# Optimization experiments

Measured on AMD Instinct MI355X. Metric: run time of the kernel, lower is better.

Reference implementation:

```python
import jax, jax.numpy as jnp
import numpy as np

HID = 64
NUM_LAYER = 3
N_OBJ = 100000
N_P1, N_P2, N_P3 = 200000, 400000, 200000
NUM_GRAPHS = 256


def _mlp(x, w1, b1, w2, b2):
    # pyg.nn.MLP([in, hid, out], norm=None): Linear -> ReLU -> Linear
    return jnp.dot(jax.nn.relu(jnp.dot(x, w1) + b1), w2) + b2


def _gather(obj, ei):
    # ei: [arity, n_atoms] object index per argument slot
    r, n = ei.shape
    g = jnp.take(obj, ei, axis=0)  # [r, n, HID]
    return jnp.moveaxis(g, 0, 1).reshape(n, r * HID)  # concat per-position embeddings


def _scatter(atom, ei, n_obj):
    # split atom embedding [n, r*HID] into r chunks and scatter-add to objects
    r, n = ei.shape
    chunks = jnp.moveaxis(atom.reshape(n, r, HID), 1, 0).reshape(r * n, HID)
    return jax.ops.segment_sum(chunks, ei.reshape(-1), num_segments=n_obj)


def _lin_init(key, fan_in, fan_out):
    kw, kb = jax.random.split(key)
    w = jax.random.normal(kw, (fan_in, fan_out), jnp.float32) / np.float32(np.sqrt(fan_in))
    b = jax.random.normal(kb, (fan_out,), jnp.float32) * 0.01
    return w, b


def setup_inputs() -> dict:
    key = jax.random.key(0)
    ks = jax.random.split(key, 16)
    inp = {}
    inp["x_obj"] = jnp.zeros((N_OBJ, 1), jnp.float32)
    inp["x_p1"] = jnp.zeros((N_P1, 1), jnp.float32)
    inp["x_p2"] = jnp.zeros((N_P2, 2), jnp.float32)
    inp["x_p3"] = jnp.zeros((N_P3, 3), jnp.float32)
    for i, (name, r) in enumerate([("p1", 1), ("p2", 2), ("p3", 3)]):
        d = HID * r
        w1, b1 = _lin_init(ks[2 * i], d, d)
        w2, b2 = _lin_init(ks[2 * i + 1], d, d)
        inp[f"w_{name}_1"], inp[f"b_{name}_1"] = w1, b1
        inp[f"w_{name}_2"], inp[f"b_{name}_2"] = w2, b2
    inp["w_u1"], inp["b_u1"] = _lin_init(ks[6], 2 * HID, 2 * HID)
    inp["w_u2"], inp["b_u2"] = _lin_init(ks[7], 2 * HID, HID)
    inp["w_r1"], inp["b_r1"] = _lin_init(ks[8], HID, 2 * HID)
    inp["w_r2"], inp["b_r2"] = _lin_init(ks[9], 2 * HID, 1)
    inp["ei_p1"] = jax.random.randint(ks[10], (1, N_P1), 0, N_OBJ, jnp.int32)
    inp["ei_p2"] = jax.random.randint(ks[11], (2, N_P2), 0, N_OBJ, jnp.int32)
    inp["ei_p3"] = jax.random.randint(ks[12], (3, N_P3), 0, N_OBJ, jnp.int32)
    inp["batch_obj"] = jnp.sort(jax.random.randint(ks[13], (N_OBJ,), 0, NUM_GRAPHS, jnp.int32))
    inp["num_graphs"] = NUM_GRAPHS
    return inp


def reference(x_obj, x_p1, x_p2, x_p3,
              w_p1_1, b_p1_1, w_p1_2, b_p1_2,
              w_p2_1, b_p2_1, w_p2_2, b_p2_2,
              w_p3_1, b_p3_1, w_p3_2, b_p3_2,
              w_u1, b_u1, w_u2, b_u2,
              w_r1, b_r1, w_r2, b_r2,
              ei_p1, ei_p2, ei_p3, batch_obj, num_graphs):
    n_obj = x_obj.shape[0]
    # encoding_layer: everything starts at zeros of size [N, F*hidden]
    obj = jnp.zeros((n_obj, x_obj.shape[1] * HID), jnp.float32)
    for _ in range(NUM_LAYER):
        # FanOutMP: gather arg-object embeddings, per-predicate MLP -> atom embeddings
        a1 = _mlp(_gather(obj, ei_p1), w_p1_1, b_p1_1, w_p1_2, b_p1_2)
        a2 = _mlp(_gather(obj, ei_p2), w_p2_1, b_p2_1, w_p2_2, b_p2_2)
        a3 = _mlp(_gather(obj, ei_p3), w_p3_1, b_p3_1, w_p3_2, b_p3_2)
        # FanInMP: split atom emb into arity chunks, scatter-add back to objects
        agg = (_scatter(a1, ei_p1, n_obj) + _scatter(a2, ei_p2, n_obj)
               + _scatter(a3, ei_p3, n_obj))
        # obj_update on cat([old_obj, aggregated])
        obj = _mlp(jnp.concatenate([obj, agg], axis=1), w_u1, b_u1, w_u2, b_u2)
    # global_add_pool + readout
    pooled = jax.ops.segment_sum(obj, batch_obj, num_segments=num_graphs)
    return _mlp(pooled, w_r1, b_r1, w_r2, b_r2).reshape(-1)
```

## Files before the change

kernel.cpp:

```cpp
#include <hip/hip_runtime.h>
#include <hip/hip_fp16.h>

typedef _Float16 h8 __attribute__((ext_vector_type(8)));
typedef float f32x4 __attribute__((ext_vector_type(4)));

__device__ __forceinline__ f32x4 mfma2(h8 ah, h8 bh, h8 bl, f32x4 c) {
    c = __builtin_amdgcn_mfma_f32_16x16x32_f16(ah, bh, c, 0, 0, 0);
    c = __builtin_amdgcn_mfma_f32_16x16x32_f16(ah, bl, c, 0, 0, 0);
    return c;
}

__launch_bounds__(256)
__global__ void wprep(const float* __restrict__ w_p1_1, const float* __restrict__ w_p1_2,
                      const float* __restrict__ w_p2_1, const float* __restrict__ w_p2_2,
                      const float* __restrict__ w_p3_1, const float* __restrict__ w_p3_2,
                      const float* __restrict__ w_u1, const float* __restrict__ w_u2,
                      _Float16* __restrict__ hb)
{
    int b = blockIdx.x;
    const float* src; int K, N, base; size_t off;
    if      (b < 16)  { src = w_p1_1; K = 64;  N = 64;  base = 0;   off = 0;      }
    else if (b < 32)  { src = w_p1_2; K = 64;  N = 64;  base = 16;  off = 8192;   }
    else if (b < 96)  { src = w_p2_1; K = 128; N = 128; base = 32;  off = 16384;  }
    else if (b < 160) { src = w_p2_2; K = 128; N = 128; base = 96;  off = 49152;  }
    else if (b < 304) { src = w_p3_1; K = 192; N = 192; base = 160; off = 81920;  }
    else if (b < 448) { src = w_p3_2; K = 192; N = 192; base = 304; off = 155648; }
    else if (b < 512) { src = w_u1;   K = 128; N = 128; base = 448; off = 229376; }
    else              { src = w_u2;   K = 128; N = 64;  base = 512; off = 262144; }
    int e = (b - base) * 256 + threadIdx.x;
    if (e < K * N) {
        int n = e / K, k = e - n * K;
        float x = src[k * N + n];
        _Float16 h = (_Float16)x;
        hb[off + e] = h;
        hb[off + (size_t)K * N + e] = (_Float16)(x - (float)h);
    }
}

__launch_bounds__(256)
__global__ void aconst_k(const float* __restrict__ b_p1_1, const float* __restrict__ w_p1_2,
                         const float* __restrict__ b_p1_2,
                         const float* __restrict__ b_p2_1, const float* __restrict__ w_p2_2,
                         const float* __restrict__ b_p2_2,
                         const float* __restrict__ b_p3_1, const float* __restrict__ w_p3_2,
                         const float* __restrict__ b_p3_2,
                         float* __restrict__ ac)
{
    int p = blockIdx.x;
    const float *b1, *w2, *b2; int D, off;
    if      (p == 0) { b1 = b_p1_1; w2 = w_p1_2; b2 = b_p1_2; D = 64;  off = 0;   }
    else if (p == 1) { b1 = b_p2_1; w2 = w_p2_2; b2 = b_p2_2; D = 128; off = 64;  }
    else             { b1 = b_p3_1; w2 = w_p3_2; b2 = b_p3_2; D = 192; off = 192; }
    int n = threadIdx.x;
    if (n < D) {
        float s = b2[n];
        for (int k = 0; k < D; ++k) {
            float h = b1[k];
            h = h > 0.f ? h : 0.f;
            s = fmaf(h, w2[k * D + n], s);
        }
        ac[off + n] = s;
    }
}

__launch_bounds__(256)
__global__ void hist_k(const int* __restrict__ ei1, const int* __restrict__ ei2,
                       const int* __restrict__ ei3, int* __restrict__ counts,
                       int n_obj, int n1, int n2, int n3)
{
    int e = blockIdx.x * 256 + threadIdx.x;
    int t1 = n1, t2 = n1 + 2 * n2, t3 = t2 + 3 * n3;
    int o, j;
    if (e < t1) { o = ei1[e]; j = 0; }
    else if (e < t2) { int x = e - t1; o = ei2[x]; j = 1 + (x >= n2 ? 1 : 0); }
    else if (e < t3) { int y = e - t2; o = ei3[y]; j = 3 + (y >= n3 ? 1 : 0) + (y >= 2 * n3 ? 1 : 0); }
    else return;
    atomicAdd(&counts[(size_t)j * n_obj + o], 1);
    atomicAdd(&counts[(size_t)6 * n_obj + o], 1);
}

__launch_bounds__(1024)
__global__ void scan_k(const int* __restrict__ deg, int* __restrict__ rowptr,
                       int* __restrict__ cursor, int n)
{
    __shared__ int buf[1024];
    __shared__ int carry_s;
    int tid = threadIdx.x;
    if (tid == 0) carry_s = 0;
    __syncthreads();
    for (int base = 0; base < n; base += 4096) {
        int idx = base + tid * 4;
        int v[4];
#pragma unroll
        for (int k = 0; k < 4; ++k) { int i = idx + k; v[k] = (i < n) ? deg[i] : 0; }
        int tsum = v[0] + v[1] + v[2] + v[3];
        buf[tid] = tsum;
        __syncthreads();
        for (int off = 1; off < 1024; off <<= 1) {
            int t = (tid >= off) ? buf[tid - off] : 0;
            __syncthreads();
            buf[tid] += t;
            __syncthreads();
        }
        int run = buf[tid] - tsum + carry_s;
#pragma unroll
        for (int k = 0; k < 4; ++k) {
            int i = idx + k;
            if (i < n) { rowptr[i] = run; cursor[i] = run; }
            run += v[k];
        }
        __syncthreads();
        if (tid == 1023) carry_s += buf[1023];
        __syncthreads();
    }
    if (tid == 0) rowptr[n] = carry_s;
}

__launch_bounds__(256)
__global__ void fill_k(const int* __restrict__ ei1, const int* __restrict__ ei2,
                       const int* __restrict__ ei3, int* __restrict__ cursor,
                       int* __restrict__ epos, int n1, int n2, int n3)
{
    int e = blockIdx.x * 256 + threadIdx.x;
    int t1 = n1, t2 = n1 + 2 * n2, t3 = t2 + 3 * n3;
    int o;
    if (e < t1) o = ei1[e];
    else if (e < t2) o = ei2[e - t1];
    else if (e < t3) o = ei3[e - t2];
    else return;
    epos[e] = atomicAdd(&cursor[o], 1);
}

__launch_bounds__(256)
__global__ void bcast_k(const int* __restrict__ counts, const float* __restrict__ ac,
                        _Float16* __restrict__ aggh, int n_obj)
{
    __shared__ float ch[384];
    int tid = threadIdx.x;
    for (int i = tid; i < 384; i += 256) ch[i] = ac[i];
    __syncthreads();
    int i = blockIdx.x * 256 + tid;
    int o = i >> 3, q = i & 7;
    if (o < n_obj) {
        float c[6];
#pragma unroll
        for (int j = 0; j < 6; ++j) c[j] = (float)counts[(size_t)j * n_obj + o];
        h8 v;
#pragma unroll
        for (int comp = 0; comp < 8; ++comp) {
            int col = 8 * q + comp;
            float s = 0.f;
#pragma unroll
            for (int j = 0; j < 6; ++j) s = fmaf(c[j], ch[j * 64 + col], s);
            v[comp] = (_Float16)s;
        }
        *(h8*)(aggh + (size_t)o * 64 + 8 * q) = v;
    }
}

template<int R, int STORE>
__device__ __forceinline__ void pred_body(
    char* smem,
    const _Float16* __restrict__ objh, const int* __restrict__ ei,
    const int* __restrict__ epos, int cbase,
    const _Float16* __restrict__ W1h, const _Float16* __restrict__ W1l,
    const float* __restrict__ B1,
    const _Float16* __restrict__ W2h, const _Float16* __restrict__ W2l,
    const float* __restrict__ B2,
    _Float16* __restrict__ aggh, _Float16* __restrict__ chunks,
    int n_atoms, int blk)
{
    constexpr int D = 64 * R;
    constexpr int KC = D / 32;
    constexpr int LDA = D + 8;
    _Float16* Ah = (_Float16*)smem;
    int* eis = (int*)(Ah + 64 * LDA);

    const int tid = threadIdx.x;
    const int wave = tid >> 6, lane = tid & 63;
    const int r = lane & 15, g = lane >> 4;
    const int a_base = blk * 64;
    const int tb = wave * R;

    for (int i = tid; i < R * 64; i += 256) {
        int s = i >> 6, a = i & 63;
        int ag = a_base + a; if (ag >= n_atoms) ag = n_atoms - 1;
        eis[i] = ei[s * n_atoms + ag];
    }
    __syncthreads();
    {
        h8 vv[2 * R];
#pragma unroll
        for (int i = 0; i < 2 * R; ++i) {
            int f = tid + 256 * i;
            int rowslot = f >> 3, c = f & 7;
            int s = rowslot >> 6, a = rowslot & 63;
            vv[i] = *(const h8*)(objh + (size_t)eis[s * 64 + a] * 64 + c * 8);
        }
#pragma unroll
        for (int i = 0; i < 2 * R; ++i) {
            int f = tid + 256 * i;
            int rowslot = f >> 3, c = f & 7;
            int s = rowslot >> 6, a = rowslot & 63;
            *(h8*)(Ah + a * LDA + s * 64 + c * 8) = vv[i];
        }
    }
    __syncthreads();

    f32x4 z = {0.f, 0.f, 0.f, 0.f};
    f32x4 acc[4][R];
#pragma unroll
    for (int rt = 0; rt < 4; ++rt)
#pragma unroll
        for (int t = 0; t < R; ++t) acc[rt][t] = z;

    {
        h8 bh[2][R], bl[2][R];
#pragma unroll
        for (int t = 0; t < R; ++t) {
            size_t wo = (size_t)((tb + t) * 16 + r) * D + g * 8;
            bh[0][t] = *(const h8*)(W1h + wo);
            bl[0][t] = *(const h8*)(W1l + wo);
        }
#pragma unroll
        for (int kc = 0; kc < KC; ++kc) {
            const int cur = kc & 1, nxt = cur ^ 1;
            if (kc + 1 < KC) {
#pragma unroll
                for (int t = 0; t < R; ++t) {
                    size_t wo = (size_t)((tb + t) * 16 + r) * D + (kc + 1) * 32 + g * 8;
                    bh[nxt][t] = *(const h8*)(W1h + wo);
                    bl[nxt][t] = *(const h8*)(W1l + wo);
                }
            }
            const int ko = kc * 32 + g * 8;
            h8 ah[4];
#pragma unroll
            for (int rt = 0; rt < 4; ++rt)
                ah[rt] = *(const h8*)(Ah + (rt * 16 + r) * LDA + ko);
// ... 71 lines not shown
                    int row = rt * 16 + g * 4 + q;
                    Ah[row * LDA + s * 64 + cc] = (_Float16)(acc[rt][t][q] + b2);
                }
        }
        __syncthreads();
#pragma unroll
        for (int p = 0; p < 2 * R; ++p) {
            int i = p * 32 + (tid >> 3);
            int s = i >> 6, a = i & 63;
            int c8 = tid & 7;
            int atom = a_base + a;
            if (atom < n_atoms) {
                int pos = epos[cbase + s * n_atoms + atom];
                *(h8*)(chunks + (size_t)pos * 64 + c8 * 8) =
                    *(const h8*)(Ah + a * LDA + s * 64 + c8 * 8);
            }
        }
    } else {
#pragma unroll
        for (int t = 0; t < R; ++t) {
            int col = (tb + t) * 16 + r;
            float b2 = B2[col];
            int s = col >> 6, cc = col & 63;
#pragma unroll
            for (int rt = 0; rt < 4; ++rt)
#pragma unroll
                for (int q = 0; q < 4; ++q) {
                    int row = rt * 16 + g * 4 + q;
                    int atom = a_base + row;
                    float v = acc[rt][t][q] + b2;
                    float v2 = __shfl_xor(v, 1);
                    if (atom < n_atoms && (r & 1) == 0) {
                        __half2 hv = __floats2half2_rn(v, v2);
                        unsafeAtomicAdd((__half2*)(aggh + (size_t)eis[s * 64 + row] * 64 + cc), hv);
                    }
                }
        }
    }
}

template<int STORE>
__launch_bounds__(256, 6)
__global__ void pred_all(const _Float16* __restrict__ objh, _Float16* __restrict__ aggh,
                         _Float16* __restrict__ chunks, const int* __restrict__ epos,
                         const int* __restrict__ ei1, const int* __restrict__ ei2,
                         const int* __restrict__ ei3,
                         const _Float16* __restrict__ hb,
                         const float* __restrict__ b_p1_1, const float* __restrict__ b_p1_2,
                         const float* __restrict__ b_p2_1, const float* __restrict__ b_p2_2,
                         const float* __restrict__ b_p3_1, const float* __restrict__ b_p3_2,
                         int n1, int n2, int n3, int nb3, int nb2)
{
    extern __shared__ char smem[];
    int b = blockIdx.x;
    if (b < nb3) {
        pred_body<3, STORE>(smem, objh, ei3, epos, n1 + 2 * n2,
                            hb + 81920, hb + 118784, b_p3_1,
                            hb + 155648, hb + 192512, b_p3_2, aggh, chunks, n3, b);
    } else if (b < nb3 + nb2) {
        pred_body<2, STORE>(smem, objh, ei2, epos, n1,
                            hb + 16384, hb + 32768, b_p2_1,
                            hb + 49152, hb + 65536, b_p2_2, aggh, chunks, n2, b - nb3);
    } else {
        pred_body<1, STORE>(smem, objh, ei1, epos, 0,
                            hb + 0, hb + 4096, b_p1_1,
                            hb + 8192, hb + 12288, b_p1_2, aggh, chunks, n1, b - nb3 - nb2);
    }
}

__launch_bounds__(256, 4)
__global__ void fanin_update(_Float16* __restrict__ objh,
                             const _Float16* __restrict__ chunks,
                             const int* __restrict__ rowptr,
                             const _Float16* __restrict__ W1h, const _Float16* __restrict__ W1l,
                             const float* __restrict__ B1,
                             const _Float16* __restrict__ W2h, const _Float16* __restrict__ W2l,
                             const float* __restrict__ B2,
                             int n_obj, int last, float* __restrict__ aggf)
{
    constexpr int LDA = 136;
    __shared__ _Float16 Ah[64 * LDA];

    const int tid = threadIdx.x;
    const int wave = tid >> 6, lane = tid & 63;
    const int r = lane & 15, g = lane >> 4;
    const int a_base = blockIdx.x * 64;

    const int o_local = tid >> 2, part = tid & 3;
    const int o = a_base + o_local;
    const bool valid = o < n_obj;
    const int b = valid ? rowptr[o] : 0;
    const int e2 = valid ? rowptr[o + 1] : 0;
    float s[16];
#pragma unroll
    for (int j = 0; j < 16; ++j) s[j] = 0.f;
    for (int i = b; i < e2; ++i) {
        const h8* cp = (const h8*)(chunks + (size_t)i * 64 + part * 16);
        h8 v0 = cp[0], v1 = cp[1];
#pragma unroll
        for (int j = 0; j < 8; ++j) { s[j] += (float)v0[j]; s[8 + j] += (float)v1[j]; }
    }
    {
        int oc = valid ? o : n_obj - 1;
        h8 u0 = *(const h8*)(objh + (size_t)oc * 64 + part * 16);
        h8 u1 = *(const h8*)(objh + (size_t)oc * 64 + part * 16 + 8);
        *(h8*)(Ah + o_local * LDA + part * 16) = u0;
        *(h8*)(Ah + o_local * LDA + part * 16 + 8) = u1;
        h8 a0, a1;
#pragma unroll
        for (int j = 0; j < 8; ++j) { a0[j] = (_Float16)s[j]; a1[j] = (_Float16)s[8 + j]; }
        *(h8*)(Ah + o_local * LDA + 64 + part * 16) = a0;
        *(h8*)(Ah + o_local * LDA + 64 + part * 16 + 8) = a1;
    }
    __syncthreads();

    f32x4 z = {0.f, 0.f, 0.f, 0.f};
    f32x4 acc[4][2];
#pragma unroll
    for (int rt = 0; rt < 4; ++rt) { acc[rt][0] = z; acc[rt][1] = z; }
    {
        h8 bh[2][2], bl[2][2];
#pragma unroll
        for (int t = 0; t < 2; ++t) {
            size_t wo = (size_t)((wave * 2 + t) * 16 + r) * 128 + g * 8;
            bh[0][t] = *(const h8*)(W1h + wo);
            bl[0][t] = *(const h8*)(W1l + wo);
        }
#pragma unroll
        for (int kc = 0; kc < 4; ++kc) {
            const int cur = kc & 1, nxt = cur ^ 1;
            if (kc + 1 < 4) {
#pragma unroll
                for (int t = 0; t < 2; ++t) {
                    size_t wo = (size_t)((wave * 2 + t) * 16 + r) * 128 + (kc + 1) * 32 + g * 8;
                    bh[nxt][t] = *(const h8*)(W1h + wo);
                    bl[nxt][t] = *(const h8*)(W1l + wo);
                }
            }
            const int ko = kc * 32 + g * 8;
            h8 ah[4];
#pragma unroll
            for (int rt = 0; rt < 4; ++rt)
                ah[rt] = *(const h8*)(Ah + (rt * 16 + r) * LDA + ko);
#pragma unroll
            for (int t = 0; t < 2; ++t)
#pragma unroll
                for (int rt = 0; rt < 4; ++rt)
                    acc[rt][t] = mfma2(ah[rt], bh[cur][t], bl[cur][t], acc[rt][t]);
        }
    }
    __syncthreads();
#pragma unroll
    for (int t = 0; t < 2; ++t) {
        int col = (wave * 2 + t) * 16 + r;
        float b1 = B1[col];
#pragma unroll
        for (int rt = 0; rt < 4; ++rt)
#pragma unroll
            for (int q = 0; q < 4; ++q) {
                int row = rt * 16 + g * 4 + q;
                float h = acc[rt][t][q] + b1;
                h = h > 0.f ? h : 0.f;
                Ah[row * LDA + col] = (_Float16)h;
            }
    }
    __syncthreads();

    f32x4 acc2[4];
#pragma unroll
    for (int rt = 0; rt < 4; ++rt) acc2[rt] = z;
    {
        h8 bh[2], bl[2];
        {
            size_t wo = (size_t)(wave * 16 + r) * 128 + g * 8;
            bh[0] = *(const h8*)(W2h + wo);
            bl[0] = *(const h8*)(W2l + wo);
        }
#pragma unroll
        for (int kc = 0; kc < 4; ++kc) {
            const int cur = kc & 1, nxt = cur ^ 1;
            if (kc + 1 < 4) {
                size_t wo = (size_t)(wave * 16 + r) * 128 + (kc + 1) * 32 + g * 8;
                bh[nxt] = *(const h8*)(W2h + wo);
                bl[nxt] = *(const h8*)(W2l + wo);
            }
            const int ko = kc * 32 + g * 8;
#pragma unroll
            for (int rt = 0; rt < 4; ++rt) {
                h8 ah = *(const h8*)(Ah + (rt * 16 + r) * LDA + ko);
                acc2[rt] = mfma2(ah, bh[cur], bl[cur], acc2[rt]);
            }
        }
    }
    {
        int col = wave * 16 + r;
        float b2 = B2[col];
#pragma unroll
        for (int rt = 0; rt < 4; ++rt)
#pragma unroll
            for (int q = 0; q < 4; ++q) {
                int row = a_base + rt * 16 + g * 4 + q;
                if (row < n_obj) {
                    float v = acc2[rt][q] + b2;
                    if (last) aggf[(size_t)row * 64 + col] = v;
                    else objh[(size_t)row * 64 + col] = (_Float16)v;
                }
            }
    }
}

template<int FIRST>
__launch_bounds__(256, 4)
__global__ void update_mfma(_Float16* __restrict__ objh, _Float16* __restrict__ aggh,
                            const _Float16* __restrict__ W1h, const _Float16* __restrict__ W1l,
                            const float* __restrict__ B1,
                            const _Float16* __restrict__ W2h, const _Float16* __restrict__ W2l,
                            const float* __restrict__ B2,
                            int n_obj, int zero_agg, int last, float* __restrict__ aggf)
{
    constexpr int LDA = 136;
    __shared__ _Float16 Ah[64 * LDA];

    const int tid = threadIdx.x;
    const int wave = tid >> 6, lane = tid & 63;
    const int r = lane & 15, g = lane >> 4;
    const int a_base = blockIdx.x * 64;

    {
#pragma unroll
        for (int i = 0; i < 4; ++i) {
            int f = tid + 256 * i;
            int a = f >> 4, c = f & 15;
            int rg = a_base + a; if (rg >= n_obj) rg = n_obj - 1;
            h8 v;
            if (c < 8) {
                if (FIRST) v = (h8)(_Float16)0.f;
                else v = *(const h8*)(objh + (size_t)rg * 64 + c * 8);
            } else {
                v = *(const h8*)(aggh + (size_t)rg * 64 + (c - 8) * 8);
            }
            *(h8*)(Ah + a * LDA + c * 8) = v;
        }
    }
    __syncthreads();

    f32x4 z = {0.f, 0.f, 0.f, 0.f};
    f32x4 acc[4][2];
#pragma unroll
    for (int rt = 0; rt < 4; ++rt) { acc[rt][0] = z; acc[rt][1] = z; }
    {
        h8 bh[2][2], bl[2][2];
#pragma unroll
        for (int t = 0; t < 2; ++t) {
            size_t wo = (size_t)((wave * 2 + t) * 16 + r) * 128 + g * 8;
            bh[0][t] = *(const h8*)(W1h + wo);
            bl[0][t] = *(const h8*)(W1l + wo);
        }
#pragma unroll
        for (int kc = 0; kc < 4; ++kc) {
            const int cur = kc & 1, nxt = cur ^ 1;
            if (kc + 1 < 4) {
#pragma unroll
                for (int t = 0; t < 2; ++t) {
                    size_t wo = (size_t)((wave * 2 + t) * 16 + r) * 128 + (kc + 1) * 32 + g * 8;
                    bh[nxt][t] = *(const h8*)(W1h + wo);
                    bl[nxt][t] = *(const h8*)(W1l + wo);
                }
            }
            const int ko = kc * 32 + g * 8;
            h8 ah[4];
#pragma unroll
            for (int rt = 0; rt < 4; ++rt)
                ah[rt] = *(const h8*)(Ah + (rt * 16 + r) * LDA + ko);
#pragma unroll
            for (int t = 0; t < 2; ++t)
#pragma unroll
                for (int rt = 0; rt < 4; ++rt)
                    acc[rt][t] = mfma2(ah[rt], bh[cur][t], bl[cur][t], acc[rt][t]);
        }
    }
    __syncthreads();
#pragma unroll
    for (int t = 0; t < 2; ++t) {
        int col = (wave * 2 + t) * 16 + r;
        float b1 = B1[col];
#pragma unroll
        for (int rt = 0; rt < 4; ++rt)
#pragma unroll
            for (int q = 0; q < 4; ++q) {
                int row = rt * 16 + g * 4 + q;
                float h = acc[rt][t][q] + b1;
                h = h > 0.f ? h : 0.f;
                Ah[row * LDA + col] = (_Float16)h;
            }
    }
    __syncthreads();

    f32x4 acc2[4];
#pragma unroll
    for (int rt = 0; rt < 4; ++rt) acc2[rt] = z;
    {
        h8 bh[2], bl[2];
        {
            size_t wo = (size_t)(wave * 16 + r) * 128 + g * 8;
            bh[0] = *(const h8*)(W2h + wo);
            bl[0] = *(const h8*)(W2l + wo);
        }
#pragma unroll
        for (int kc = 0; kc < 4; ++kc) {
            const int cur = kc & 1, nxt = cur ^ 1;
            if (kc + 1 < 4) {
                size_t wo = (size_t)(wave * 16 + r) * 128 + (kc + 1) * 32 + g * 8;
                bh[nxt] = *(const h8*)(W2h + wo);
                bl[nxt] = *(const h8*)(W2l + wo);
            }
            const int ko = kc * 32 + g * 8;
#pragma unroll
            for (int rt = 0; rt < 4; ++rt) {
                h8 ah = *(const h8*)(Ah + (rt * 16 + r) * LDA + ko);
                acc2[rt] = mfma2(ah, bh[cur], bl[cur], acc2[rt]);
            }
        }
    }
    __syncthreads();
    {
        int col = wave * 16 + r;
        float b2 = B2[col];
#pragma unroll
        for (int rt = 0; rt < 4; ++rt)
#pragma unroll
            for (int q = 0; q < 4; ++q) {
                int row = a_base + rt * 16 + g * 4 + q;
                if (row < n_obj) {
                    float v = acc2[rt][q] + b2;
                    if (last) aggf[(size_t)row * 64 + col] = v;
                    else objh[(size_t)row * 64 + col] = (_Float16)v;
                }
            }
    }
    if (zero_agg) {
        h8 zz = (h8)(_Float16)0.f;
#pragma unroll
        for (int i = 0; i < 2; ++i) {
            int f = tid + 256 * i;
            int a = f >> 3, q = f & 7;
            int rg = a_base + a;
            if (rg < n_obj) *(h8*)(aggh + (size_t)rg * 64 + q * 8) = zz;
        }
    }
}

__global__ void pool_kernel(const float* __restrict__ obj, const int* __restrict__ batch,
                            float* __restrict__ pooled, int n_obj)
{
    int i = blockIdx.x * 256 + threadIdx.x;
    int row = i >> 4, q = i & 15;
    if (row < n_obj) {
        float4 v = ((const float4*)obj)[(size_t)row * 16 + q];
        int g = batch[row];
        float* p = pooled + g * 64 + 4 * q;
        atomicAdd(p + 0, v.x);
        atomicAdd(p + 1, v.y);
        atomicAdd(p + 2, v.z);
        atomicAdd(p + 3, v.w);
    }
}

__launch_bounds__(128)
__global__ void readout_kernel(const float* __restrict__ pooled,
                               const float* __restrict__ w1, const float* __restrict__ b1,
                               const float* __restrict__ w2, const float* __restrict__ b2,
                               float* __restrict__ out)
{
    int g = blockIdx.x, c = threadIdx.x;
    __shared__ float xs[64];
    __shared__ float red[2];
    if (c < 64) xs[c] = pooled[g * 64 + c];
    __syncthreads();
    float h = b1[c];
#pragma unroll
    for (int k = 0; k < 64; ++k) h = fmaf(xs[k], w1[k * 128 + c], h);
    float v = fmaxf(h, 0.f) * w2[c];
#pragma unroll
    for (int off = 32; off > 0; off >>= 1) v += __shfl_down(v, off);
    if ((c & 63) == 0) red[c >> 6] = v;
    __syncthreads();
    if (c == 0) out[g] = red[0] + red[1] + b2[0];
}

static inline size_t align_up(size_t x) { return (x + 255) & ~(size_t)255; }

extern "C" void kernel_launch(void* const* d_in, const int* in_sizes, int n_in,
                              void* d_out, int out_size, void* d_ws, size_t ws_size,
                              hipStream_t stream)
{
    const float* w_p1_1 = (const float*)d_in[4];
    const float* b_p1_1 = (const float*)d_in[5];
    const float* w_p1_2 = (const float*)d_in[6];
    const float* b_p1_2 = (const float*)d_in[7];
    const float* w_p2_1 = (const float*)d_in[8];
    const float* b_p2_1 = (const float*)d_in[9];
    const float* w_p2_2 = (const float*)d_in[10];
    const float* b_p2_2 = (const float*)d_in[11];
    const float* w_p3_1 = (const float*)d_in[12];
    const float* b_p3_1 = (const float*)d_in[13];
    const float* w_p3_2 = (const float*)d_in[14];
    const float* b_p3_2 = (const float*)d_in[15];
    const float* w_u1 = (const float*)d_in[16];
    const float* b_u1 = (const float*)d_in[17];
    const float* w_u2 = (const float*)d_in[18];
    const float* b_u2 = (const float*)d_in[19];
    const float* w_r1 = (const float*)d_in[20];
    const float* b_r1 = (const float*)d_in[21];
    const float* w_r2 = (const float*)d_in[22];
    const float* b_r2 = (const float*)d_in[23];
    const int* ei_p1 = (const int*)d_in[24];
    const int* ei_p2 = (const int*)d_in[25];
    const int* ei_p3 = (const int*)d_in[26];
    const int* batch = (const int*)d_in[27];

    const int n_obj = in_sizes[0];
    const int n_p1 = in_sizes[24];
    const int n_p2 = in_sizes[25] / 2;
    const int n_p3 = in_sizes[26] / 3;
    const int E = n_p1 + 2 * n_p2 + 3 * n_p3;

    char* base = (char*)d_ws;
    size_t off = 0;
    _Float16* objh = (_Float16*)(base + off); off = align_up(off + (size_t)n_obj * 64 * 2);
    _Float16* aggh = (_Float16*)(base + off); off = align_up(off + (size_t)n_obj * 64 * 2);
    float* aggf = (float*)(base + off);       off = align_up(off + (size_t)n_obj * 64 * 4);
    float* pooled = (float*)(base + off);     off = align_up(off + (size_t)out_size * 64 * 4);
    _Float16* hb = (_Float16*)(base + off);   off = align_up(off + (size_t)278528 * 2);
    int* counts = (int*)(base + off);         off = align_up(off + (size_t)7 * n_obj * 4);
    int* deg = counts + (size_t)6 * n_obj;
    int* rowptr = (int*)(base + off);         off = align_up(off + ((size_t)n_obj + 1) * 4);
    int* cursor = (int*)(base + off);         off = align_up(off + (size_t)n_obj * 4);
    int* epos = (int*)(base + off);           off = align_up(off + (size_t)E * 4);
    _Float16* chunks = (_Float16*)(base + off); off = align_up(off + (size_t)E * 64 * 2);
    const bool csr_ok = off <= ws_size;
    float* ac = pooled;

    const int nb3 = (n_p3 + 63) / 64, nb2 = (n_p2 + 63) / 64, nb1 = (n_p1 + 63) / 64;
    const int pred_smem = 64 * (192 + 8) * 2 + 3 * 64 * 4;

    wprep<<<544, 256, 0, stream>>>(w_p1_1, w_p1_2, w_p2_1, w_p2_2, w_p3_1, w_p3_2,
                                   w_u1, w_u2, hb);
    aconst_k<<<3, 256, 0, stream>>>(b_p1_1, w_p1_2, b_p1_2, b_p2_1, w_p2_2, b_p2_2,
                                    b_p3_1, w_p3_2, b_p3_2, ac);
    hipMemsetAsync(counts, 0, (size_t)7 * n_obj * sizeof(int), stream);
    hist_k<<<(E + 255) / 256, 256, 0, stream>>>(ei_p1, ei_p2, ei_p3, counts,
                                                n_obj, n_p1, n_p2, n_p3);
    if (csr_ok) {
        scan_k<<<1, 1024, 0, stream>>>(deg, rowptr, cursor, n_obj);
        fill_k<<<(E + 255) / 256, 256, 0, stream>>>(ei_p1, ei_p2, ei_p3, cursor, epos,
                                                    n_p1, n_p2, n_p3);
    }
    bcast_k<<<((size_t)n_obj * 8 + 255) / 256, 256, 0, stream>>>(counts, ac, aggh, n_obj);
    update_mfma<1><<<(n_obj + 63) / 64, 256, 0, stream>>>(
        objh, aggh, hb + 229376, hb + 245760, b_u1, hb + 262144, hb + 270336, b_u2,
        n_obj, csr_ok ? 0 : 1, 0, aggf);
    if (csr_ok) {
        for (int l = 1; l < 3; ++l) {
            pred_all<1><<<nb3 + nb2 + nb1, 256, pred_smem, stream>>>(
                objh, aggh, chunks, epos, ei_p1, ei_p2, ei_p3, hb,
                b_p1_1, b_p1_2, b_p2_1, b_p2_2, b_p3_1, b_p3_2,
                n_p1, n_p2, n_p3, nb3, nb2);
            fanin_update<<<(n_obj + 63) / 64, 256, 0, stream>>>(
                objh, chunks, rowptr,
                hb + 229376, hb + 245760, b_u1, hb + 262144, hb + 270336, b_u2,
                n_obj, l == 2 ? 1 : 0, aggf);
        }
    } else {
        for (int l = 1; l < 3; ++l) {
            pred_all<0><<<nb3 + nb2 + nb1, 256, pred_smem, stream>>>(
                objh, aggh, chunks, epos, ei_p1, ei_p2, ei_p3, hb,
                b_p1_1, b_p1_2, b_p2_1, b_p2_2, b_p3_1, b_p3_2,
                n_p1, n_p2, n_p3, nb3, nb2);
            update_mfma<0><<<(n_obj + 63) / 64, 256, 0, stream>>>(
                objh, aggh, hb + 229376, hb + 245760, b_u1, hb + 262144, hb + 270336, b_u2,
                n_obj, l < 2 ? 1 : 0, l == 2 ? 1 : 0, aggf);
        }
    }
    hipMemsetAsync(pooled, 0, (size_t)out_size * 64 * sizeof(float), stream);
    pool_kernel<<<((size_t)n_obj * 16 + 255) / 256, 256, 0, stream>>>(aggf, batch, pooled, n_obj);
    readout_kernel<<<out_size, 128, 0, stream>>>(pooled, w_r1, b_r1, w_r2, b_r2, (float*)d_out);
}
```

Before: 1.416 ms.

## Merge setup kernels, parallelize CSR scan, fuse bcast into first update

Combines weight prep, bias-constant computation and the histogram into one launch. The single-block scan is replaced with a three-stage multi-block scan. The first-layer aggregate broadcast is computed directly inside the update kernel, so aggh is no longer written and read back. The fanin gather loop is also unrolled by two. These changes cut launch count, the serial scan latency and one intermediate memory round trip, but add more kernel variants to maintain.

```diff
diff --git a/kernel.cpp b/kernel.cpp
--- a/kernel.cpp
+++ b/kernel.cpp
@@ -11,109 +11,124 @@
 }
 
 __launch_bounds__(256)
-__global__ void wprep(const float* __restrict__ w_p1_1, const float* __restrict__ w_p1_2,
-                      const float* __restrict__ w_p2_1, const float* __restrict__ w_p2_2,
-                      const float* __restrict__ w_p3_1, const float* __restrict__ w_p3_2,
-                      const float* __restrict__ w_u1, const float* __restrict__ w_u2,
-                      _Float16* __restrict__ hb)
+__global__ void setup_k(const float* __restrict__ w_p1_1, const float* __restrict__ w_p1_2,
+                        const float* __restrict__ w_p2_1, const float* __restrict__ w_p2_2,
+                        const float* __restrict__ w_p3_1, const float* __restrict__ w_p3_2,
+                        const float* __restrict__ w_u1, const float* __restrict__ w_u2,
+                        _Float16* __restrict__ hb,
+                        const float* __restrict__ b_p1_1, const float* __restrict__ b_p1_2,
+                        const float* __restrict__ b_p2_1, const float* __restrict__ b_p2_2,
+                        const float* __restrict__ b_p3_1, const float* __restrict__ b_p3_2,
+                        float* __restrict__ ac,
+                        const int* __restrict__ ei1, const int* __restrict__ ei2,
+                        const int* __restrict__ ei3, int* __restrict__ counts,
+                        int n_obj, int n1, int n2, int n3)
 {
     int b = blockIdx.x;
-    const float* src; int K, N, base; size_t off;
-    if      (b < 16)  { src = w_p1_1; K = 64;  N = 64;  base = 0;   off = 0;      }
-    else if (b < 32)  { src = w_p1_2; K = 64;  N = 64;  base = 16;  off = 8192;   }
-    else if (b < 96)  { src = w_p2_1; K = 128; N = 128; base = 32;  off = 16384;  }
-    else if (b < 160) { src = w_p2_2; K = 128; N = 128; base = 96;  off = 49152;  }
-    else if (b < 304) { src = w_p3_1; K = 192; N = 192; base = 160; off = 81920;  }
-    else if (b < 448) { src = w_p3_2; K = 192; N = 192; base = 304; off = 155648; }
-    else if (b < 512) { src = w_u1;   K = 128; N = 128; base = 448; off = 229376; }
-    else              { src = w_u2;   K = 128; N = 64;  base = 512; off = 262144; }
-    int e = (b - base) * 256 + threadIdx.x;
-    if (e < K * N) {
-        int n = e / K, k = e - n * K;
-        float x = src[k * N + n];
-        _Float16 h = (_Float16)x;
-        hb[off + e] = h;
-        hb[off + (size_t)K * N + e] = (_Float16)(x - (float)h);
+    if (b < 544) {
+        const float* src; int K, N, base; size_t off;
+        if      (b < 16)  { src = w_p1_1; K = 64;  N = 64;  base = 0;   off = 0;      }
+        else if (b < 32)  { src = w_p1_2; K = 64;  N = 64;  base = 16;  off = 8192;   }
+        else if (b < 96)  { src = w_p2_1; K = 128; N = 128; base = 32;  off = 16384;  }
+        else if (b < 160) { src = w_p2_2; K = 128; N = 128; base = 96;  off = 49152;  }
+        else if (b < 304) { src = w_p3_1; K = 192; N = 192; base = 160; off = 81920;  }
+        else if (b < 448) { src = w_p3_2; K = 192; N = 192; base = 304; off = 155648; }
+        else if (b < 512) { src = w_u1;   K = 128; N = 128; base = 448; off = 229376; }
+        else              { src = w_u2;   K = 128; N = 64;  base = 512; off = 262144; }
+        int e = (b - base) * 256 + threadIdx.x;
+        if (e < K * N) {
+            int n = e / K, k = e - n * K;
+            float x = src[k * N + n];
+            _Float16 h = (_Float16)x;
+            hb[off + e] = h;
+            hb[off + (size_t)K * N + e] = (_Float16)(x - (float)h);
+        }
+    } else if (b < 547) {
+        int p = b - 544;
+        const float *b1, *w2, *b2; int D, off;
+        if      (p == 0) { b1 = b_p1_1; w2 = w_p1_2; b2 = b_p1_2; D = 64;  off = 0;   }
+        else if (p == 1) { b1 = b_p2_1; w2 = w_p2_2; b2 = b_p2_2; D = 128; off = 64;  }
+        else             { b1 = b_p3_1; w2 = w_p3_2; b2 = b_p3_2; D = 192; off = 192; }
+        int n = threadIdx.x;
+        if (n < D) {
+            float s = b2[n];
+            for (int k = 0; k < D; ++k) {
+                float h = b1[k];
+                h = h > 0.f ? h : 0.f;
+                s = fmaf(h, w2[k * D + n], s);
+            }
+            ac[off + n] = s;
+        }
+    } else {
+        int e = (b - 547) * 256 + threadIdx.x;
+        int t1 = n1, t2 = n1 + 2 * n2, t3 = t2 + 3 * n3;
+        int o, j;
+        if (e < t1) { o = ei1[e]; j = 0; }
+        else if (e < t2) { int x = e - t1; o = ei2[x]; j = 1 + (x >= n2 ? 1 : 0); }
+        else if (e < t3) { int y = e - t2; o = ei3[y]; j = 3 + (y >= n3 ? 1 : 0) + (y >= 2 * n3 ? 1 : 0); }
+        else return;
+        atomicAdd(&counts[(size_t)j * n_obj + o], 1);
+        atomicAdd(&counts[(size_t)6 * n_obj + o], 1);
     }
 }
 
 __launch_bounds__(256)
-__global__ void aconst_k(const float* __restrict__ b_p1_1, const float* __restrict__ w_p1_2,
-                         const float* __restrict__ b_p1_2,
-                         const float* __restrict__ b_p2_1, const float* __restrict__ w_p2_2,
-                         const float* __restrict__ b_p2_2,
-                         const float* __restrict__ b_p3_1, const float* __restrict__ w_p3_2,
-                         const float* __restrict__ b_p3_2,
-                         float* __restrict__ ac)
-{
-    int p = blockIdx.x;
-    const float *b1, *w2, *b2; int D, off;
-    if      (p == 0) { b1 = b_p1_1; w2 = w_p1_2; b2 = b_p1_2; D = 64;  off = 0;   }
-    else if (p == 1) { b1 = b_p2_1; w2 = w_p2_2; b2 = b_p2_2; D = 128; off = 64;  }
-    else             { b1 = b_p3_1; w2 = w_p3_2; b2 = b_p3_2; D = 192; off = 192; }
-    int n = threadIdx.x;
-    if (n < D) {
-        float s = b2[n];
-        for (int k = 0; k < D; ++k) {
-            float h = b1[k];
-            h = h > 0.f ? h : 0.f;
-            s = fmaf(h, w2[k * D + n], s);
-        }
-        ac[off + n] = s;
-    }
+__global__ void scan1_k(const int* __restrict__ deg, int* __restrict__ rowptr,
+                        int* __restrict__ bsum, int n)
+{
+    __shared__ int buf[256];
+    int tid = threadIdx.x;
+    int base = blockIdx.x * 1024 + tid * 4;
+    int v[4];
+#pragma unroll
+    for (int k = 0; k < 4; ++k) { int i = base + k; v[k] = (i < n) ? deg[i] : 0; }
+    int tsum = v[0] + v[1] + v[2] + v[3];
+    buf[tid] = tsum;
+    __syncthreads();
+    for (int off = 1; off < 256; off <<= 1) {
+        int t = (tid >= off) ? buf[tid - off] : 0;
+        __syncthreads();
+        buf[tid] += t;
+        __syncthreads();
+    }
+    int run = buf[tid] - tsum;
+#pragma unroll
+    for (int k = 0; k < 4; ++k) {
+        int i = base + k;
+        if (i < n) rowptr[i] = run;
+        run += v[k];
+    }
+    if (tid == 255) bsum[blockIdx.x] = buf[255];
 }
 
 __launch_bounds__(256)
-__global__ void hist_k(const int* __restrict__ ei1, const int* __restrict__ ei2,
-                       const int* __restrict__ ei3, int* __restrict__ counts,
-                       int n_obj, int n1, int n2, int n3)
-{
-    int e = blockIdx.x * 256 + threadIdx.x;
-    int t1 = n1, t2 = n1 + 2 * n2, t3 = t2 + 3 * n3;
-    int o, j;
-    if (e < t1) { o = ei1[e]; j = 0; }
-    else if (e < t2) { int x = e - t1; o = ei2[x]; j = 1 + (x >= n2 ? 1 : 0); }
-    else if (e < t3) { int y = e - t2; o = ei3[y]; j = 3 + (y >= n3 ? 1 : 0) + (y >= 2 * n3 ? 1 : 0); }
-    else return;
-    atomicAdd(&counts[(size_t)j * n_obj + o], 1);
-    atomicAdd(&counts[(size_t)6 * n_obj + o], 1);
-}
-
-__launch_bounds__(1024)
-__global__ void scan_k(const int* __restrict__ deg, int* __restrict__ rowptr,
-                       int* __restrict__ cursor, int n)
-{
-    __shared__ int buf[1024];
-    __shared__ int carry_s;
+__global__ void scan2_k(int* __restrict__ bsum, int* __restrict__ rowptr, int n, int nb)
+{
+    __shared__ int buf[256];
     int tid = threadIdx.x;
-    if (tid == 0) carry_s = 0;
-    __syncthreads();
-    for (int base = 0; base < n; base += 4096) {
-        int idx = base + tid * 4;
-        int v[4];
-#pragma unroll
-        for (int k = 0; k < 4; ++k) { int i = idx + k; v[k] = (i < n) ? deg[i] : 0; }
-        int tsum = v[0] + v[1] + v[2] + v[3];
-        buf[tid] = tsum;
+    int v = (tid < nb) ? bsum[tid] : 0;
+    buf[tid] = v;
+    __syncthreads();
+    for (int off = 1; off < 256; off <<= 1) {
+        int t = (tid >= off) ? buf[tid - off] : 0;
         __syncthreads();
-        for (int off = 1; off < 1024; off <<= 1) {
-            int t = (tid >= off) ? buf[tid - off] : 0;
-            __syncthreads();
-            buf[tid] += t;
-            __syncthreads();
-        }
-        int run = buf[tid] - tsum + carry_s;
-#pragma unroll
-        for (int k = 0; k < 4; ++k) {
-            int i = idx + k;
-            if (i < n) { rowptr[i] = run; cursor[i] = run; }
-            run += v[k];
-        }
+        buf[tid] += t;
         __syncthreads();
-        if (tid == 1023) carry_s += buf[1023];
-        __syncthreads();
-    }
-    if (tid == 0) rowptr[n] = carry_s;
+    }
+    if (tid < nb) bsum[tid] = buf[tid] - v;
+    if (tid == 255) rowptr[n] = buf[255];
+}
+
+__launch_bounds__(256)
+__global__ void scan3_k(int* __restrict__ rowptr, int* __restrict__ cursor,
+                        const int* __restrict__ bsum, int n)
+{
+    int i = blockIdx.x * 256 + threadIdx.x;
+    if (i < n) {
+        int r = rowptr[i] + bsum[i >> 10];
+        rowptr[i] = r;
+        cursor[i] = r;
+    }
 }
 
 __launch_bounds__(256)
@@ -155,6 +170,199 @@
             v[comp] = (_Float16)s;
         }
         *(h8*)(aggh + (size_t)o * 64 + 8 * q) = v;
+    }
+}
+
+__device__ __forceinline__ void update_tail(
+    _Float16* __restrict__ Ah, _Float16* __restrict__ objh,
+    const _Float16* __restrict__ W1h, const _Float16* __restrict__ W1l,
+    const float* __restrict__ B1,
+    const _Float16* __restrict__ W2h, const _Float16* __restrict__ W2l,
+    const float* __restrict__ B2,
+    int n_obj, int a_base, int last, float* __restrict__ aggf)
+{
+    constexpr int LDA = 136;
+    const int tid = threadIdx.x;
+    const int wave = tid >> 6, lane = tid & 63;
+    const int r = lane & 15, g = lane >> 4;
+
+    f32x4 z = {0.f, 0.f, 0.f, 0.f};
+    f32x4 acc[4][2];
+#pragma unroll
+    for (int rt = 0; rt < 4; ++rt) { acc[rt][0] = z; acc[rt][1] = z; }
+    {
+        h8 bh[2][2], bl[2][2];
+#pragma unroll
+        for (int t = 0; t < 2; ++t) {
+            size_t wo = (size_t)((wave * 2 + t) * 16 + r) * 128 + g * 8;
+            bh[0][t] = *(const h8*)(W1h + wo);
+            bl[0][t] = *(const h8*)(W1l + wo);
+        }
+#pragma unroll
+        for (int kc = 0; kc < 4; ++kc) {
+            const int cur = kc & 1, nxt = cur ^ 1;
+            if (kc + 1 < 4) {
+#pragma unroll
+                for (int t = 0; t < 2; ++t) {
+                    size_t wo = (size_t)((wave * 2 + t) * 16 + r) * 128 + (kc + 1) * 32 + g * 8;
+                    bh[nxt][t] = *(const h8*)(W1h + wo);
+                    bl[nxt][t] = *(const h8*)(W1l + wo);
+                }
+            }
+            const int ko = kc * 32 + g * 8;
+            h8 ah[4];
+#pragma unroll
+            for (int rt = 0; rt < 4; ++rt)
+                ah[rt] = *(const h8*)(Ah + (rt * 16 + r) * LDA + ko);
+#pragma unroll
+            for (int t = 0; t < 2; ++t)
+#pragma unroll
+                for (int rt = 0; rt < 4; ++rt)
+                    acc[rt][t] = mfma2(ah[rt], bh[cur][t], bl[cur][t], acc[rt][t]);
+        }
+    }
+    __syncthreads();
+#pragma unroll
+    for (int t = 0; t < 2; ++t) {
+        int col = (wave * 2 + t) * 16 + r;
+        float b1 = B1[col];
+#pragma unroll
+        for (int rt = 0; rt < 4; ++rt)
+#pragma unroll
+            for (int q = 0; q < 4; ++q) {
+                int row = rt * 16 + g * 4 + q;
+                float h = acc[rt][t][q] + b1;
+                h = h > 0.f ? h : 0.f;
+                Ah[row * LDA + col] = (_Float16)h;
+            }
+    }
+    __syncthreads();
+
+    f32x4 acc2[4];
+#pragma unroll
+    for (int rt = 0; rt < 4; ++rt) acc2[rt] = z;
+    {
+        h8 bh[2], bl[2];
+        {
+            size_t wo = (size_t)(wave * 16 + r) * 128 + g * 8;
+            bh[0] = *(const h8*)(W2h + wo);
+            bl[0] = *(const h8*)(W2l + wo);
+        }
+#pragma unroll
+        for (int kc = 0; kc < 4; ++kc) {
+            const int cur = kc & 1, nxt = cur ^ 1;
+            if (kc + 1 < 4) {
+                size_t wo = (size_t)(wave * 16 + r) * 128 + (kc + 1) * 32 + g * 8;
+                bh[nxt] = *(const h8*)(W2h + wo);
+                bl[nxt] = *(const h8*)(W2l + wo);
+            }
+            const int ko = kc * 32 + g * 8;
+#pragma unroll
+            for (int rt = 0; rt < 4; ++rt) {
+                h8 ah = *(const h8*)(Ah + (rt * 16 + r) * LDA + ko);
+                acc2[rt] = mfma2(ah, bh[cur], bl[cur], acc2[rt]);
+            }
+        }
+    }
+    {
+        int col = wave * 16 + r;
+        float b2 = B2[col];
+#pragma unroll
+        for (int rt = 0; rt < 4; ++rt)
+#pragma unroll
+            for (int q = 0; q < 4; ++q) {
+                int row = a_base + rt * 16 + g * 4 + q;
+                if (row < n_obj) {
+                    float v = acc2[rt][q] + b2;
+                    if (last) aggf[(size_t)row * 64 + col] = v;
+                    else objh[(size_t)row * 64 + col] = (_Float16)v;
+                }
+            }
+    }
+}
+
+__launch_bounds__(256, 4)
+__global__ void update0_bcast(_Float16* __restrict__ objh,
+                              const int* __restrict__ counts, const float* __restrict__ ac,
+                              const _Float16* __restrict__ W1h, const _Float16* __restrict__ W1l,
+                              const float* __restrict__ B1,
+                              const _Float16* __restrict__ W2h, const _Float16* __restrict__ W2l,
+                              const float* __restrict__ B2, int n_obj)
+{
+    constexpr int LDA = 136;
+    __shared__ _Float16 Ah[64 * LDA];
+    __shared__ float ch[384];
+    const int tid = threadIdx.x;
+    const int a_base = blockIdx.x * 64;
+
+    for (int i = tid; i < 384; i += 256) ch[i] = ac[i];
+    __syncthreads();
+#pragma unroll
+    for (int i = 0; i < 4; ++i) {
+        int f = tid + 256 * i;
+        int a = f >> 4, c = f & 15;
+        int rg = a_base + a; if (rg >= n_obj) rg = n_obj - 1;
+        h8 v;
+        if (c < 8) {
+            v = (h8)(_Float16)0.f;
+        } else {
+            float cc[6];
+#pragma unroll
+            for (int j = 0; j < 6; ++j) cc[j] = (float)counts[(size_t)j * n_obj + rg];
+#pragma unroll
+            for (int comp = 0; comp < 8; ++comp) {
+                int col = (c - 8) * 8 + comp;
+                float s = 0.f;
+#pragma unroll
+                for (int j = 0; j < 6; ++j) s = fmaf(cc[j], ch[j * 64 + col], s);
+                v[comp] = (_Float16)s;
+            }
+        }
+        *(h8*)(Ah + a * LDA + c * 8) = v;
+    }
+    __syncthreads();
+    update_tail(Ah, objh, W1h, W1l, B1, W2h, W2l, B2, n_obj, a_base, 0, nullptr);
+}
+
+template<int FIRST>
+__launch_bounds__(256, 4)
+__global__ void update_mfma(_Float16* __restrict__ objh, _Float16* __restrict__ aggh,
+                            const _Float16* __restrict__ W1h, const _Float16* __restrict__ W1l,
+                            const float* __restrict__ B1,
+                            const _Float16* __restrict__ W2h, const _Float16* __restrict__ W2l,
+                            const float* __restrict__ B2,
+                            int n_obj, int zero_agg, int last, float* __restrict__ aggf)
+{
+    constexpr int LDA = 136;
+    __shared__ _Float16 Ah[64 * LDA];
+    const int tid = threadIdx.x;
+    const int a_base = blockIdx.x * 64;
+#pragma unroll
+    for (int i = 0; i < 4; ++i) {
+        int f = tid + 256 * i;
+        int a = f >> 4, c = f & 15;
+        int rg = a_base + a; if (rg >= n_obj) rg = n_obj - 1;
+        h8 v;
+        if (c < 8) {
+            if (FIRST) v = (h8)(_Float16)0.f;
+            else v = *(const h8*)(objh + (size_t)rg * 64 + c * 8);
+        } else {
+            v = *(const h8*)(aggh + (size_t)rg * 64 + (c - 8) * 8);
+        }
+        *(h8*)(Ah + a * LDA + c * 8) = v;
+    }
+    __syncthreads();
+    update_tail(Ah, objh, W1h, W1l, B1, W2h, W2l, B2, n_obj, a_base, last, aggf);
+    if (zero_agg) {
+        __syncthreads();
+        h8 zz = (h8)(_Float16)0.f;
+#pragma unroll
+        for (int i = 0; i < 2; ++i) {
+            int f = tid + 256 * i;
+            int a = f >> 3, q = f & 7;
+            int rg = a_base + a;
+            if (rg < n_obj) *(h8*)(aggh + (size_t)rg * 64 + q * 8) = zz;
+        }
     }
 }
 
@@ -392,8 +600,6 @@
     __shared__ _Float16 Ah[64 * LDA];
 
     const int tid = threadIdx.x;
-    const int wave = tid >> 6, lane = tid & 63;
-    const int r = lane & 15, g = lane >> 4;
     const int a_base = blockIdx.x * 64;
 
     const int o_local = tid >> 2, part = tid & 3;
@@ -404,11 +610,22 @@
     float s[16];
 #pragma unroll
     for (int j = 0; j < 16; ++j) s[j] = 0.f;
-    for (int i = b; i < e2; ++i) {
-        const h8* cp = (const h8*)(chunks + (size_t)i * 64 + part * 16);
-        h8 v0 = cp[0], v1 = cp[1];
-#pragma unroll
-        for (int j = 0; j < 8; ++j) { s[j] += (float)v0[j]; s[8 + j] += (float)v1[j]; }
+    int i = b;
+    for (; i + 2 <= e2; i += 2) {
+        const h8* c0 = (const h8*)(chunks + (size_t)i * 64 + part * 16);
+        const h8* c1 = (const h8*)(chunks + (size_t)(i + 1) * 64 + part * 16);
+        h8 a0 = c0[0], a1 = c0[1], d0 = c1[0], d1 = c1[1];
+#pragma unroll
+        for (int j = 0; j < 8; ++j) {
+            s[j] += (float)a0[j] + (float)d0[j];
+            s[8 + j] += (float)a1[j] + (float)d1[j];
+        }
+    }
+    if (i < e2) {
+        const h8* c0 = (const h8*)(chunks + (size_t)i * 64 + part * 16);
+        h8 a0 = c0[0], a1 = c0[1];
+#pragma unroll
+        for (int j = 0; j < 8; ++j) { s[j] += (float)a0[j]; s[8 + j] += (float)a1[j]; }
     }
     {
         int oc = valid ? o : n_obj - 1;
@@ -423,241 +640,7 @@
         *(h8*)(Ah + o_local * LDA + 64 + part * 16 + 8) = a1;
     }
     __syncthreads();
-
-    f32x4 z = {0.f, 0.f, 0.f, 0.f};
-    f32x4 acc[4][2];
-#pragma unroll
-    for (int rt = 0; rt < 4; ++rt) { acc[rt][0] = z; acc[rt][1] = z; }
-    {
-        h8 bh[2][2], bl[2][2];
-#pragma unroll
-        for (int t = 0; t < 2; ++t) {
-            size_t wo = (size_t)((wave * 2 + t) * 16 + r) * 128 + g * 8;
-            bh[0][t] = *(const h8*)(W1h + wo);
-            bl[0][t] = *(const h8*)(W1l + wo);
-        }
-#pragma unroll
-        for (int kc = 0; kc < 4; ++kc) {
-            const int cur = kc & 1, nxt = cur ^ 1;
-            if (kc + 1 < 4) {
-#pragma unroll
-                for (int t = 0; t < 2; ++t) {
-                    size_t wo = (size_t)((wave * 2 + t) * 16 + r) * 128 + (kc + 1) * 32 + g * 8;
-                    bh[nxt][t] = *(const h8*)(W1h + wo);
-                    bl[nxt][t] = *(const h8*)(W1l + wo);
-                }
-            }
-            const int ko = kc * 32 + g * 8;
-            h8 ah[4];
-#pragma unroll
-            for (int rt = 0; rt < 4; ++rt)
-                ah[rt] = *(const h8*)(Ah + (rt * 16 + r) * LDA + ko);
-#pragma unroll
-            for (int t = 0; t < 2; ++t)
-#pragma unroll
-                for (int rt = 0; rt < 4; ++rt)
-                    acc[rt][t] = mfma2(ah[rt], bh[cur][t], bl[cur][t], acc[rt][t]);
-        }
-    }
-    __syncthreads();
-#pragma unroll
-    for (int t = 0; t < 2; ++t) {
-        int col = (wave * 2 + t) * 16 + r;
-        float b1 = B1[col];
-#pragma unroll
-        for (int rt = 0; rt < 4; ++rt)
-#pragma unroll
-            for (int q = 0; q < 4; ++q) {
-                int row = rt * 16 + g * 4 + q;
-                float h = acc[rt][t][q] + b1;
-                h = h > 0.f ? h : 0.f;
-                Ah[row * LDA + col] = (_Float16)h;
-            }
-    }
-    __syncthreads();
-
-    f32x4 acc2[4];
-#pragma unroll
-    for (int rt = 0; rt < 4; ++rt) acc2[rt] = z;
-    {
-        h8 bh[2], bl[2];
-        {
-            size_t wo = (size_t)(wave * 16 + r) * 128 + g * 8;
-            bh[0] = *(const h8*)(W2h + wo);
-            bl[0] = *(const h8*)(W2l + wo);
-        }
-#pragma unroll
-        for (int kc = 0; kc < 4; ++kc) {
-            const int cur = kc & 1, nxt = cur ^ 1;
-            if (kc + 1 < 4) {
-                size_t wo = (size_t)(wave * 16 + r) * 128 + (kc + 1) * 32 + g * 8;
-                bh[nxt] = *(const h8*)(W2h + wo);
-                bl[nxt] = *(const h8*)(W2l + wo);
-            }
-            const int ko = kc * 32 + g * 8;
-#pragma unroll
-            for (int rt = 0; rt < 4; ++rt) {
-                h8 ah = *(const h8*)(Ah + (rt * 16 + r) * LDA + ko);
-                acc2[rt] = mfma2(ah, bh[cur], bl[cur], acc2[rt]);
-            }
-        }
-    }
-    {
-        int col = wave * 16 + r;
-        float b2 = B2[col];
-#pragma unroll
-        for (int rt = 0; rt < 4; ++rt)
-#pragma unroll
-            for (int q = 0; q < 4; ++q) {
-                int row = a_base + rt * 16 + g * 4 + q;
-                if (row < n_obj) {
-                    float v = acc2[rt][q] + b2;
-                    if (last) aggf[(size_t)row * 64 + col] = v;
-                    else objh[(size_t)row * 64 + col] = (_Float16)v;
-                }
-            }
-    }
-}
-
-template<int FIRST>
-__launch_bounds__(256, 4)
-__global__ void update_mfma(_Float16* __restrict__ objh, _Float16* __restrict__ aggh,
-                            const _Float16* __restrict__ W1h, const _Float16* __restrict__ W1l,
-                            const float* __restrict__ B1,
-                            const _Float16* __restrict__ W2h, const _Float16* __restrict__ W2l,
-                            const float* __restrict__ B2,
-                            int n_obj, int zero_agg, int last, float* __restrict__ aggf)
-{
-    constexpr int LDA = 136;
-    __shared__ _Float16 Ah[64 * LDA];
-
-    const int tid = threadIdx.x;
-    const int wave = tid >> 6, lane = tid & 63;
-    const int r = lane & 15, g = lane >> 4;
-    const int a_base = blockIdx.x * 64;
-
-    {
-#pragma unroll
-        for (int i = 0; i < 4; ++i) {
-            int f = tid + 256 * i;
-            int a = f >> 4, c = f & 15;
-            int rg = a_base + a; if (rg >= n_obj) rg = n_obj - 1;
-            h8 v;
-            if (c < 8) {
-                if (FIRST) v = (h8)(_Float16)0.f;
-                else v = *(const h8*)(objh + (size_t)rg * 64 + c * 8);
-            } else {
-                v = *(const h8*)(aggh + (size_t)rg * 64 + (c - 8) * 8);
-            }
-            *(h8*)(Ah + a * LDA + c * 8) = v;
-        }
-    }
-    __syncthreads();
-
-    f32x4 z = {0.f, 0.f, 0.f, 0.f};
-    f32x4 acc[4][2];
-#pragma unroll
-    for (int rt = 0; rt < 4; ++rt) { acc[rt][0] = z; acc[rt][1] = z; }
-    {
-        h8 bh[2][2], bl[2][2];
-#pragma unroll
-        for (int t = 0; t < 2; ++t) {
-            size_t wo = (size_t)((wave * 2 + t) * 16 + r) * 128 + g * 8;
-            bh[0][t] = *(const h8*)(W1h + wo);
-            bl[0][t] = *(const h8*)(W1l + wo);
-        }
-#pragma unroll
-        for (int kc = 0; kc < 4; ++kc) {
-            const int cur = kc & 1, nxt = cur ^ 1;
-            if (kc + 1 < 4) {
-#pragma unroll
-                for (int t = 0; t < 2; ++t) {
-                    size_t wo = (size_t)((wave * 2 + t) * 16 + r) * 128 + (kc + 1) * 32 + g * 8;
-                    bh[nxt][t] = *(const h8*)(W1h + wo);
-                    bl[nxt][t] = *(const h8*)(W1l + wo);
-                }
-            }
-            const int ko = kc * 32 + g * 8;
-            h8 ah[4];
-#pragma unroll
-            for (int rt = 0; rt < 4; ++rt)
-                ah[rt] = *(const h8*)(Ah + (rt * 16 + r) * LDA + ko);
-#pragma unroll
-            for (int t = 0; t < 2; ++t)
-#pragma unroll
-                for (int rt = 0; rt < 4; ++rt)
-                    acc[rt][t] = mfma2(ah[rt], bh[cur][t], bl[cur][t], acc[rt][t]);
-        }
-    }
-    __syncthreads();
-#pragma unroll
-    for (int t = 0; t < 2; ++t) {
-        int col = (wave * 2 + t) * 16 + r;
-        float b1 = B1[col];
-#pragma unroll
-        for (int rt = 0; rt < 4; ++rt)
-#pragma unroll
-            for (int q = 0; q < 4; ++q) {
-                int row = rt * 16 + g * 4 + q;
-                float h = acc[rt][t][q] + b1;
-                h = h > 0.f ? h : 0.f;
-                Ah[row * LDA + col] = (_Float16)h;
-            }
-    }
-    __syncthreads();
-
-    f32x4 acc2[4];
-#pragma unroll
-    for (int rt = 0; rt < 4; ++rt) acc2[rt] = z;
-    {
-        h8 bh[2], bl[2];
-        {
-            size_t wo = (size_t)(wave * 16 + r) * 128 + g * 8;
-            bh[0] = *(const h8*)(W2h + wo);
-            bl[0] = *(const h8*)(W2l + wo);
-        }
-#pragma unroll
-        for (int kc = 0; kc < 4; ++kc) {
-            const int cur = kc & 1, nxt = cur ^ 1;
-            if (kc + 1 < 4) {
-                size_t wo = (size_t)(wave * 16 + r) * 128 + (kc + 1) * 32 + g * 8;
-                bh[nxt] = *(const h8*)(W2h + wo);
-                bl[nxt] = *(const h8*)(W2l + wo);
-            }
-            const int ko = kc * 32 + g * 8;
-#pragma unroll
-            for (int rt = 0; rt < 4; ++rt) {
-                h8 ah = *(const h8*)(Ah + (rt * 16 + r) * LDA + ko);
-                acc2[rt] = mfma2(ah, bh[cur], bl[cur], acc2[rt]);
-            }
-        }
-    }
-    __syncthreads();
-    {
-        int col = wave * 16 + r;
-        float b2 = B2[col];
-#pragma unroll
-        for (int rt = 0; rt < 4; ++rt)
-#pragma unroll
-            for (int q = 0; q < 4; ++q) {
-                int row = a_base + rt * 16 + g * 4 + q;
-                if (row < n_obj) {
-                    float v = acc2[rt][q] + b2;
-                    if (last) aggf[(size_t)row * 64 + col] = v;
-                    else objh[(size_t)row * 64 + col] = (_Float16)v;
-                }
-            }
-    }
-    if (zero_agg) {
-        h8 zz = (h8)(_Float16)0.f;
-#pragma unroll
-        for (int i = 0; i < 2; ++i) {
-            int f = tid + 256 * i;
-            int a = f >> 3, q = f & 7;
-            int rg = a_base + a;
-            if (rg < n_obj) *(h8*)(aggh + (size_t)rg * 64 + q * 8) = zz;
-        }
-    }
+    update_tail(Ah, objh, W1h, W1l, B1, W2h, W2l, B2, n_obj, a_base, last, aggf);
 }
 
 __global__ void pool_kernel(const float* __restrict__ obj, const int* __restrict__ batch,
@@ -746,6 +729,7 @@
     int* deg = counts + (size_t)6 * n_obj;
     int* rowptr = (int*)(base + off);         off = align_up(off + ((size_t)n_obj + 1) * 4);
     int* cursor = (int*)(base + off);         off = align_up(off + (size_t)n_obj * 4);
+    int* bsum = (int*)(base + off);           off = align_up(off + 256 * 4);
     int* epos = (int*)(base + off);           off = align_up(off + (size_t)E * 4);
     _Float16* chunks = (_Float16*)(base + off); off = align_up(off + (size_t)E * 64 * 2);
     const bool csr_ok = off <= ws_size;
@@ -753,24 +737,22 @@
 
     const int nb3 = (n_p3 + 63) / 64, nb2 = (n_p2 + 63) / 64, nb1 = (n_p1 + 63) / 64;
     const int pred_smem = 64 * (192 + 8) * 2 + 3 * 64 * 4;
-
-    wprep<<<544, 256, 0, stream>>>(w_p1_1, w_p1_2, w_p2_1, w_p2_2, w_p3_1, w_p3_2,
-                                   w_u1, w_u2, hb);
-    aconst_k<<<3, 256, 0, stream>>>(b_p1_1, w_p1_2, b_p1_2, b_p2_1, w_p2_2, b_p2_2,
-                                    b_p3_1, w_p3_2, b_p3_2, ac);
+    const int nbs = (n_obj + 1023) / 1024;
+
     hipMemsetAsync(counts, 0, (size_t)7 * n_obj * sizeof(int), stream);
-    hist_k<<<(E + 255) / 256, 256, 0, stream>>>(ei_p1, ei_p2, ei_p3, counts,
-                                                n_obj, n_p1, n_p2, n_p3);
+    setup_k<<<547 + (E + 255) / 256, 256, 0, stream>>>(
+        w_p1_1, w_p1_2, w_p2_1, w_p2_2, w_p3_1, w_p3_2, w_u1, w_u2, hb,
+        b_p1_1, b_p1_2, b_p2_1, b_p2_2, b_p3_1, b_p3_2, ac,
+        ei_p1, ei_p2, ei_p3, counts, n_obj, n_p1, n_p2, n_p3);
     if (csr_ok) {
-        scan_k<<<1, 1024, 0, stream>>>(deg, rowptr, cursor, n_obj);
+        scan1_k<<<nbs, 256, 0, stream>>>(deg, rowptr, bsum, n_obj);
+        scan2_k<<<1, 256, 0, stream>>>(bsum, rowptr, n_obj, nbs);
+        scan3_k<<<(n_obj + 255) / 256, 256, 0, stream>>>(rowptr, cursor, bsum, n_obj);
         fill_k<<<(E + 255) / 256, 256, 0, stream>>>(ei_p1, ei_p2, ei_p3, cursor, epos,
                                                     n_p1, n_p2, n_p3);
-    }
-    bcast_k<<<((size_t)n_obj * 8 + 255) / 256, 256, 0, stream>>>(counts, ac, aggh, n_obj);
-    update_mfma<1><<<(n_obj + 63) / 64, 256, 0, stream>>>(
-        objh, aggh, hb + 229376, hb + 245760, b_u1, hb + 262144, hb + 270336, b_u2,
-        n_obj, csr_ok ? 0 : 1, 0, aggf);
-    if (csr_ok) {
+        update0_bcast<<<(n_obj + 63) / 64, 256, 0, stream>>>(
+            objh, counts, ac, hb + 229376, hb + 245760, b_u1,
+            hb + 262144, hb + 270336, b_u2, n_obj);
         for (int l = 1; l < 3; ++l) {
             pred_all<1><<<nb3 + nb2 + nb1, 256, pred_smem, stream>>>(
                 objh, aggh, chunks, epos, ei_p1, ei_p2, ei_p3, hb,
@@ -782,6 +764,10 @@
                 n_obj, l == 2 ? 1 : 0, aggf);
         }
     } else {
+        bcast_k<<<((size_t)n_obj * 8 + 255) / 256, 256, 0, stream>>>(counts, ac, aggh, n_obj);
+        update_mfma<1><<<(n_obj + 63) / 64, 256, 0, stream>>>(
+            objh, aggh, hb + 229376, hb + 245760, b_u1, hb + 262144, hb + 270336, b_u2,
+            n_obj, 1, 0, aggf);
         for (int l = 1; l < 3; ++l) {
             pred_all<0><<<nb3 + nb2 + nb1, 256, pred_smem, stream>>>(
                 objh, aggh, chunks, epos, ei_p1, ei_p2, ei_p3, hb,
```

After: 1.303 ms. 8.0% less time.
